# Kernel tuning notes

Measured on AMD Instinct MI355X. Metric: run time of the kernel, lower is better.

The kernel has to match this reference:

```python
import jax, jax.numpy as jnp
import numpy as np

NUM_CLASSES = 1000
NUM_NEIGHBOURS = 200
SIGMA = 10.0
GAUSS_CONST = 1.0 / (2.0 * SIGMA ** 2)


def setup_inputs() -> dict:
    key = jax.random.key(0)
    k1, k2, k3 = jax.random.split(key, 3)
    B, D, C = 512, 512, 100000
    features = jax.random.normal(k1, (B, D), dtype=jnp.float32)
    centres = jax.random.normal(k2, (C, D), dtype=jnp.float32)
    centre_labels = jax.random.randint(k3, (C,), 0, NUM_CLASSES)
    weight = jnp.zeros((C,), dtype=jnp.float32)
    return {"features": features, "centres": centres,
            "centre_labels": centre_labels, "weight": weight}


def _knn(features, centres, k):
    # squared euclidean distances [B, C] without materializing [B, C, D]
    f2 = jnp.sum(features * features, axis=1, keepdims=True)      # [B,1]
    c2 = jnp.sum(centres * centres, axis=1)                        # [C]
    d2 = f2 + c2[None, :] - 2.0 * features @ centres.T             # [B,C]
    _, idx = jax.lax.top_k(-d2, k)                                 # smallest k
    return idx                                                     # [B,k]


def reference(features, centres, centre_labels, weight):
    B = features.shape[0]
    K = NUM_NEIGHBOURS
    nbr = _knn(features, centres, K)                               # [B,K] int
    gathered = centres[nbr]                                        # [B,K,D]
    d2 = jnp.sum((features[:, None, :] - gathered) ** 2, axis=-1)  # [B,K]
    kernel_weights = jnp.exp(weight)                               # [C]
    d = jnp.exp(-d2 * GAUSS_CONST) * kernel_weights[nbr]           # [B,K]
    nbr_labels = centre_labels[nbr]                                # [B,K]
    rows = jnp.arange(B)[:, None]
    p = jnp.zeros((B, NUM_CLASSES), dtype=d.dtype).at[rows, nbr_labels].add(d)
    p = jnp.where(p == 0, 1e-10, p)
    p = p / jnp.sum(p, axis=1, keepdims=True)
    return jnp.log(p)
```

## Files before the change

### kernel.cpp

```cpp
#include <hip/hip_runtime.h>
#include <hip/hip_fp16.h>
#include <math.h>
#include <stdint.h>

#define D_DIM    512
#define NCLS     1000
#define KSEL     200
#define NBINS    1024
#define CAND_MAX 2048
#define GCONST   0.005
#define MARGIN   2.0f

typedef short s8v __attribute__((ext_vector_type(8)));
typedef float f4v __attribute__((ext_vector_type(4)));

#define GLOAD_LDS16(gp, lp) __builtin_amdgcn_global_load_lds( \
    (const __attribute__((address_space(1))) void*)(gp),      \
    (__attribute__((address_space(3))) void*)(lp), 16, 0, 0)

static __device__ __forceinline__ unsigned short f2bf(float x) {
    unsigned u = __float_as_uint(x);
    return (unsigned short)((u + 0x7FFFu + ((u >> 16) & 1u)) >> 16);
}

__global__ __launch_bounds__(256)
void convertF(const float* __restrict__ F, unsigned short* __restrict__ Fb,
              float* __restrict__ f2)
{
    __shared__ float red[256];
    const int r = blockIdx.x, t = threadIdx.x;
    float2 v = *(const float2*)(F + (size_t)r * D_DIM + t * 2);
    ushort2 o; o.x = f2bf(v.x); o.y = f2bf(v.y);
    *(ushort2*)(Fb + (size_t)r * D_DIM + t * 2) = o;
    red[t] = v.x * v.x + v.y * v.y;
    __syncthreads();
    for (int off = 128; off > 0; off >>= 1) {
        if (t < off) red[t] += red[t + off];
        __syncthreads();
    }
    if (t == 0) f2[r] = red[0];
}

__global__ __launch_bounds__(256)
void convertC(const float* __restrict__ C, unsigned short* __restrict__ Cb,
              float* __restrict__ c2, int N)
{
    const int lane   = threadIdx.x & 63;
    const int wglob  = (int)((blockIdx.x * 256 + threadIdx.x) >> 6);
    const int nwaves = (int)((gridDim.x * 256) >> 6);
    for (int row = wglob; row < N; row += nwaves) {
        const float* rp = C + (size_t)row * D_DIM;
        float4 a = *(const float4*)(rp + lane * 8);
        float4 b = *(const float4*)(rp + lane * 8 + 4);
        float s = a.x*a.x + a.y*a.y + a.z*a.z + a.w*a.w
                + b.x*b.x + b.y*b.y + b.z*b.z + b.w*b.w;
        uint4 o;
        o.x = (unsigned)f2bf(a.x) | ((unsigned)f2bf(a.y) << 16);
        o.y = (unsigned)f2bf(a.z) | ((unsigned)f2bf(a.w) << 16);
        o.z = (unsigned)f2bf(b.x) | ((unsigned)f2bf(b.y) << 16);
        o.w = (unsigned)f2bf(b.z) | ((unsigned)f2bf(b.w) << 16);
        *(uint4*)(Cb + (size_t)row * D_DIM + lane * 8) = o;
#pragma unroll
        for (int off = 32; off > 0; off >>= 1) s += __shfl_down(s, off, 64);
        if (lane == 0) c2[row] = s;
    }
}

__global__ __launch_bounds__(256)
void mfma_gemm(const unsigned short* __restrict__ Fb,
               const unsigned short* __restrict__ Cb,
               __half* __restrict__ Sm, int N)
{
    __shared__ short As[128 * 64];
    __shared__ short Bs[128 * 64];
    const int t    = threadIdx.x;
    const int lane = t & 63;
    const int w    = t >> 6;
    const int wm   = w >> 1, wn = w & 1;
    const int m0   = blockIdx.y * 128;
    const int n0   = blockIdx.x * 128;
    const int lrow = lane >> 3;
    const int lcol = (lane & 7) * 8;

    f4v acc[4][4];
#pragma unroll
    for (int i = 0; i < 4; ++i)
#pragma unroll
        for (int j = 0; j < 4; ++j) acc[i][j] = (f4v){0.f, 0.f, 0.f, 0.f};

    const int quad = lane >> 4;
    const int col  = lane & 15;

    for (int k0 = 0; k0 < D_DIM; k0 += 64) {
#pragma unroll
        for (int cc = 0; cc < 4; ++cc) {
            int ch = w * 4 + cc;
            const unsigned short* ga =
                Fb + (size_t)(m0 + ch * 8 + lrow) * D_DIM + k0 + lcol;
            GLOAD_LDS16(ga, &As[ch * 512]);
            const unsigned short* gb =
                Cb + (size_t)(n0 + ch * 8 + lrow) * D_DIM + k0 + lcol;
            GLOAD_LDS16(gb, &Bs[ch * 512]);
        }
        __syncthreads();
#pragma unroll
        for (int kk = 0; kk < 2; ++kk) {
            const int kof = kk * 32 + quad * 8;
            s8v a[4], b[4];
#pragma unroll
            for (int i = 0; i < 4; ++i)
                a[i] = *(s8v*)&As[(wm * 64 + i * 16 + col) * 64 + kof];
#pragma unroll
            for (int j = 0; j < 4; ++j)
                b[j] = *(s8v*)&Bs[(wn * 64 + j * 16 + col) * 64 + kof];
#pragma unroll
            for (int i = 0; i < 4; ++i)
#pragma unroll
                for (int j = 0; j < 4; ++j)
                    acc[i][j] = __builtin_amdgcn_mfma_f32_16x16x32_bf16(
                        a[i], b[j], acc[i][j], 0, 0, 0);
        }
        __syncthreads();
    }

#pragma unroll
    for (int i = 0; i < 4; ++i) {
        int m = m0 + wm * 64 + i * 16 + quad * 4;
#pragma unroll
        for (int j = 0; j < 4; ++j) {
            int n = n0 + wn * 64 + j * 16 + col;
            if (n < N) {
#pragma unroll
                for (int v = 0; v < 4; ++v)
                    Sm[(size_t)(m + v) * N + n] = __float2half(acc[i][j][v]);
            }
        }
    }
}

__global__ __launch_bounds__(1024)
void fused_select(const __half* __restrict__ Sm, const float* __restrict__ f2,
                  const float* __restrict__ c2,
                  const float* __restrict__ F, const float* __restrict__ C,
                  const int* __restrict__ labels, const float* __restrict__ weight,
                  float* __restrict__ out, int N)
{
    __shared__ unsigned hist[NBINS];
    __shared__ float    fs[D_DIM];
    __shared__ int      idxs[CAND_MAX];
    __shared__ double   dists[CAND_MAX];
    __shared__ float    p[NCLS];
    __shared__ float    red[1024];
    __shared__ unsigned scanbuf[256];
    __shared__ float    sT;
    __shared__ unsigned scnt;

    const int r = blockIdx.x, t = threadIdx.x;
    for (int b = t; b < NBINS; b += 1024) hist[b] = 0u;
    for (int c = t; c < NCLS; c += 1024) p[c] = 0.f;
    for (int k = t; k < D_DIM; k += 1024) fs[k] = F[(size_t)r * D_DIM + k];
    if (t == 0) { sT = 1e30f; scnt = 0u; }
    __syncthreads();

    const float fr = f2[r];
    const __half* srow = Sm + (size_t)r * N;

    for (int j = t * 4; j < N; j += 4096) {
        float4 cc = *(const float4*)(c2 + j);
        float2 s01 = __half22float2(*(const __half2*)(srow + j));
        float2 s23 = __half22float2(*(const __half2*)(srow + j + 2));
        float d2v[4] = { fr + cc.x - 2.f * s01.x, fr + cc.y - 2.f * s01.y,
                         fr + cc.z - 2.f * s23.x, fr + cc.w - 2.f * s23.y };
#pragma unroll
        for (int e = 0; e < 4; ++e) {
            int b = (int)(d2v[e] * 0.5f);
            b = b < 0 ? 0 : (b > NBINS - 1 ? NBINS - 1 : b);
            atomicAdd(&hist[b], 1u);
        }
    }
    __syncthreads();

    if (t < 256) {
        unsigned loc[NBINS / 256];
        unsigned s = 0;
#pragma unroll
        for (int i = 0; i < NBINS / 256; ++i) {
            loc[i] = hist[t * (NBINS / 256) + i];
            s += loc[i];
        }
        scanbuf[t] = s;
        __syncthreads();
        unsigned pre = 0;
        for (int u = 0; u < t; ++u) pre += scanbuf[u];
        if (pre < KSEL && pre + s >= KSEL) {
            unsigned cum = pre;
            int b = NBINS - 1;
#pragma unroll
            for (int i = 0; i < NBINS / 256; ++i) {
                cum += loc[i];
                if (cum >= KSEL) { b = t * (NBINS / 256) + i; break; }
            }
            sT = 2.0f * (float)(b + 1) + MARGIN;
        }
    } else {
        __syncthreads();
    }
    __syncthreads();
    const float Tr = sT;

    for (int j = t * 4; j < N; j += 4096) {
        float4 cc = *(const float4*)(c2 + j);
        float2 s01 = __half22float2(*(const __half2*)(srow + j));
        float2 s23 = __half22float2(*(const __half2*)(srow + j + 2));
        float d2v[4] = { fr + cc.x - 2.f * s01.x, fr + cc.y - 2.f * s01.y,
                         fr + cc.z - 2.f * s23.x, fr + cc.w - 2.f * s23.y };
#pragma unroll
        for (int e = 0; e < 4; ++e) {
            if (d2v[e] <= Tr) {
                unsigned pos = atomicAdd(&scnt, 1u);
                if (pos < CAND_MAX) idxs[pos] = j + e;
            }
        }
    }
    __syncthreads();
    int Nc = (int)scnt;
    if (Nc > CAND_MAX) Nc = CAND_MAX;

    {
        const int wv = t >> 6, lane = t & 63;
        for (int i = wv; i < Nc; i += 16) {
            int ci = idxs[i];
            const float* cp = C + (size_t)ci * D_DIM;
            float4 a  = *(const float4*)(cp + lane * 8);
            float4 b  = *(const float4*)(cp + lane * 8 + 4);
            float4 fa = *(const float4*)(fs + lane * 8);
            float4 fb = *(const float4*)(fs + lane * 8 + 4);
            double d0 = (double)fa.x - (double)a.x;
            double d1 = (double)fa.y - (double)a.y;
            double d2 = (double)fa.z - (double)a.z;
            double d3 = (double)fa.w - (double)a.w;
            double d4 = (double)fb.x - (double)b.x;
            double d5 = (double)fb.y - (double)b.y;
            double d6 = (double)fb.z - (double)b.z;
            double d7 = (double)fb.w - (double)b.w;
            double acc = d0*d0 + d1*d1 + d2*d2 + d3*d3
                       + d4*d4 + d5*d5 + d6*d6 + d7*d7;
#pragma unroll
            for (int off = 32; off > 0; off >>= 1)
                acc += __shfl_down(acc, off, 64);
            if (lane == 0) dists[i] = acc;
        }
    }
    __syncthreads();

    int ksel = KSEL < Nc ? KSEL : Nc;
    for (int i = t; i < Nc; i += 1024) {
        double di = dists[i];
        int    ii = idxs[i];
        int rank = 0;
        for (int j = 0; j < Nc; ++j) {
            double dj = dists[j];
            rank += (dj < di) || (dj == di && idxs[j] < ii);
        }
        if (rank < ksel) {
            double wgt = exp(-di * GCONST) * exp((double)weight[ii]);
            atomicAdd(&p[labels[ii]], (float)wgt);
        }
    }
    __syncthreads();

    float s = 0.f;
    for (int c = t; c < NCLS; c += 1024) {
        float v = p[c];
        if (v == 0.f) v = 1e-10f;
        p[c] = v;
        s += v;
    }
    red[t] = s;
    __syncthreads();
    for (int o = 512; o > 0; o >>= 1) {
        if (t < o) red[t] += red[t + o];
        __syncthreads();
    }
    float total = red[0];
    for (int c = t; c < NCLS; c += 1024)
        out[(size_t)r * NCLS + c] = logf(p[c] / total);
}

extern "C" void kernel_launch(void* const* d_in, const int* in_sizes, int n_in,
                              void* d_out, int out_size, void* d_ws, size_t ws_size,
                              hipStream_t stream)
{
    const float* features = (const float*)d_in[0];
    const float* centres  = (const float*)d_in[1];
    const int*   labels   = (const int*)d_in[2];
    const float* weight   = (const float*)d_in[3];
    const int B = in_sizes[0] / D_DIM;
    const int N = in_sizes[2];
    float* out = (float*)d_out;

    uint8_t* w = (uint8_t*)d_ws;
    size_t off = 0;
    auto alloc = [&](size_t bytes) -> uint8_t* {
        uint8_t* ptr = w + off;
        off = (off + bytes + 255) & ~(size_t)255;
        return ptr;
    };
    float*          f2 = (float*)alloc((size_t)B * 4);
    float*          c2 = (float*)alloc((size_t)N * 4);
    unsigned short* Fb = (unsigned short*)alloc((size_t)B * D_DIM * 2);
    unsigned short* Cb = (unsigned short*)alloc((size_t)N * D_DIM * 2);
    __half*         Sm = (__half*)alloc((size_t)B * N * 2);
    (void)ws_size;

    convertF<<<B, 256, 0, stream>>>(features, Fb, f2);
    convertC<<<1024, 256, 0, stream>>>(centres, Cb, c2, N);

    dim3 ggrid((N + 127) / 128, B / 128);
    mfma_gemm<<<ggrid, 256, 0, stream>>>(Fb, Cb, Sm, N);

    fused_select<<<B, 1024, 0, stream>>>(Sm, f2, c2, features, centres,
                                         labels, weight, out, N);
}
```

Before: 494.8 us.

## Swizzle GEMM LDS tiles, stage output through LDS, widen select loads

XOR-swizzles the bf16 A/B tiles in shared memory to avoid bank conflicts on the MFMA operand reads. Stages the fp16 score tile through shared memory so each thread writes 16-byte coalesced rows instead of scattered 2-byte stores. Also widens the per-thread loads in the histogram and candidate passes of the select kernel to 8 halves. The wide loads need N to be a multiple of 8 (100000 is); otherwise the tail read would run past the row.

```diff
diff --git a/kernel.cpp b/kernel.cpp
--- a/kernel.cpp
+++ b/kernel.cpp
@@ -71,8 +71,9 @@
                const unsigned short* __restrict__ Cb,
                __half* __restrict__ Sm, int N)
 {
-    __shared__ short As[128 * 64];
-    __shared__ short Bs[128 * 64];
+    __shared__ short smem[2 * 128 * 64];
+    short* As = smem;
+    short* Bs = smem + 128 * 64;
     const int t    = threadIdx.x;
     const int lane = t & 63;
     const int w    = t >> 6;
@@ -80,7 +81,7 @@
     const int m0   = blockIdx.y * 128;
     const int n0   = blockIdx.x * 128;
     const int lrow = lane >> 3;
-    const int lcol = (lane & 7) * 8;
+    const int koct = ((lane & 7) ^ (lrow & 7)) * 8;
 
     f4v acc[4][4];
 #pragma unroll
@@ -96,23 +97,28 @@
         for (int cc = 0; cc < 4; ++cc) {
             int ch = w * 4 + cc;
             const unsigned short* ga =
-                Fb + (size_t)(m0 + ch * 8 + lrow) * D_DIM + k0 + lcol;
+                Fb + (size_t)(m0 + ch * 8 + lrow) * D_DIM + k0 + koct;
             GLOAD_LDS16(ga, &As[ch * 512]);
             const unsigned short* gb =
-                Cb + (size_t)(n0 + ch * 8 + lrow) * D_DIM + k0 + lcol;
+                Cb + (size_t)(n0 + ch * 8 + lrow) * D_DIM + k0 + koct;
             GLOAD_LDS16(gb, &Bs[ch * 512]);
         }
         __syncthreads();
 #pragma unroll
         for (int kk = 0; kk < 2; ++kk) {
-            const int kof = kk * 32 + quad * 8;
             s8v a[4], b[4];
 #pragma unroll
-            for (int i = 0; i < 4; ++i)
-                a[i] = *(s8v*)&As[(wm * 64 + i * 16 + col) * 64 + kof];
-#pragma unroll
-            for (int j = 0; j < 4; ++j)
-                b[j] = *(s8v*)&Bs[(wn * 64 + j * 16 + col) * 64 + kof];
+            for (int i = 0; i < 4; ++i) {
+                int row = wm * 64 + i * 16 + col;
+                int slot = (kk * 4 + quad) ^ (col & 7);
+                a[i] = *(s8v*)&As[row * 64 + slot * 8];
+            }
+#pragma unroll
+            for (int j = 0; j < 4; ++j) {
+                int row = wn * 64 + j * 16 + col;
+                int slot = (kk * 4 + quad) ^ (col & 7);
+                b[j] = *(s8v*)&Bs[row * 64 + slot * 8];
+            }
 #pragma unroll
             for (int i = 0; i < 4; ++i)
 #pragma unroll
@@ -123,17 +129,33 @@
         __syncthreads();
     }
 
+    __half* Cs = (__half*)smem;
 #pragma unroll
     for (int i = 0; i < 4; ++i) {
-        int m = m0 + wm * 64 + i * 16 + quad * 4;
 #pragma unroll
         for (int j = 0; j < 4; ++j) {
-            int n = n0 + wn * 64 + j * 16 + col;
-            if (n < N) {
-#pragma unroll
-                for (int v = 0; v < 4; ++v)
-                    Sm[(size_t)(m + v) * N + n] = __float2half(acc[i][j][v]);
-            }
+#pragma unroll
+            for (int v = 0; v < 4; ++v) {
+                int ml = wm * 64 + i * 16 + quad * 4 + v;
+                int nl = wn * 64 + j * 16 + col;
+                int slot = ((nl >> 3) ^ (ml & 7));
+                Cs[ml * 128 + slot * 8 + (nl & 7)] = __float2half(acc[i][j][v]);
+            }
+        }
+    }
+    __syncthreads();
+#pragma unroll
+    for (int it = 0; it < 8; ++it) {
+        int idx = it * 256 + t;
+        int row = idx >> 4;
+        int oct = idx & 15;
+        int n   = n0 + oct * 8;
+        const __half* src = &Cs[row * 128 + ((oct ^ (row & 7)) * 8)];
+        __half* dst = Sm + (size_t)(m0 + row) * N + n;
+        if (n + 7 < N) {
+            *(uint4*)dst = *(const uint4*)src;
+        } else if (n < N) {
+            for (int e = 0; e < 8 && n + e < N; ++e) dst[e] = src[e];
         }
     }
 }
@@ -165,14 +187,20 @@
     const float fr = f2[r];
     const __half* srow = Sm + (size_t)r * N;
 
-    for (int j = t * 4; j < N; j += 4096) {
-        float4 cc = *(const float4*)(c2 + j);
-        float2 s01 = __half22float2(*(const __half2*)(srow + j));
-        float2 s23 = __half22float2(*(const __half2*)(srow + j + 2));
-        float d2v[4] = { fr + cc.x - 2.f * s01.x, fr + cc.y - 2.f * s01.y,
-                         fr + cc.z - 2.f * s23.x, fr + cc.w - 2.f * s23.y };
-#pragma unroll
-        for (int e = 0; e < 4; ++e) {
+    for (int j = t * 8; j < N; j += 8192) {
+        uint4 sv = *(const uint4*)(srow + j);
+        float4 ca = *(const float4*)(c2 + j);
+        float4 cb = *(const float4*)(c2 + j + 4);
+        float2 s0 = __half22float2(*(__half2*)&sv.x);
+        float2 s1 = __half22float2(*(__half2*)&sv.y);
+        float2 s2 = __half22float2(*(__half2*)&sv.z);
+        float2 s3 = __half22float2(*(__half2*)&sv.w);
+        float d2v[8] = { fr + ca.x - 2.f * s0.x, fr + ca.y - 2.f * s0.y,
+                         fr + ca.z - 2.f * s1.x, fr + ca.w - 2.f * s1.y,
+                         fr + cb.x - 2.f * s2.x, fr + cb.y - 2.f * s2.y,
+                         fr + cb.z - 2.f * s3.x, fr + cb.w - 2.f * s3.y };
+#pragma unroll
+        for (int e = 0; e < 8; ++e) {
             int b = (int)(d2v[e] * 0.5f);
             b = b < 0 ? 0 : (b > NBINS - 1 ? NBINS - 1 : b);
             atomicAdd(&hist[b], 1u);
@@ -208,14 +236,20 @@
     __syncthreads();
     const float Tr = sT;
 
-    for (int j = t * 4; j < N; j += 4096) {
-        float4 cc = *(const float4*)(c2 + j);
-        float2 s01 = __half22float2(*(const __half2*)(srow + j));
-        float2 s23 = __half22float2(*(const __half2*)(srow + j + 2));
-        float d2v[4] = { fr + cc.x - 2.f * s01.x, fr + cc.y - 2.f * s01.y,
-                         fr + cc.z - 2.f * s23.x, fr + cc.w - 2.f * s23.y };
-#pragma unroll
-        for (int e = 0; e < 4; ++e) {
+    for (int j = t * 8; j < N; j += 8192) {
+        uint4 sv = *(const uint4*)(srow + j);
+        float4 ca = *(const float4*)(c2 + j);
+        float4 cb = *(const float4*)(c2 + j + 4);
+        float2 s0 = __half22float2(*(__half2*)&sv.x);
+        float2 s1 = __half22float2(*(__half2*)&sv.y);
+        float2 s2 = __half22float2(*(__half2*)&sv.z);
+        float2 s3 = __half22float2(*(__half2*)&sv.w);
+        float d2v[8] = { fr + ca.x - 2.f * s0.x, fr + ca.y - 2.f * s0.y,
+                         fr + ca.z - 2.f * s1.x, fr + ca.w - 2.f * s1.y,
+                         fr + cb.x - 2.f * s2.x, fr + cb.y - 2.f * s2.y,
+                         fr + cb.z - 2.f * s3.x, fr + cb.w - 2.f * s3.y };
+#pragma unroll
+        for (int e = 0; e < 8; ++e) {
             if (d2v[e] <= Tr) {
                 unsigned pos = atomicAdd(&scnt, 1u);
                 if (pos < CAND_MAX) idxs[pos] = j + e;
```

New measurement: 491.3 us. About the same (-0.7%).
